# Kernel tuning notes

Measured on AMD Instinct MI355X. Metric: run time of the kernel, lower is better.

Reference implementation:

```python
import jax, jax.numpy as jnp
import numpy as np

B, T, S, H, V, E = 32, 256, 32, 512, 128, 512


def setup_inputs() -> dict:
    key = jax.random.key(0)
    ks = jax.random.split(key, 20)
    f = lambda i, shape: jax.random.normal(ks[i], shape, jnp.float32) * 0.05
    return dict(
        embedding=f(0, (V, H)),
        scope_enc=f(1, (B, S, H)),
        spec_enc=f(2, (B, E)),
        W_init=f(3, (H, E)), b_init=jnp.zeros((H,), jnp.float32),
        W_ih=f(4, (3 * H, 2 * H)), W_hh=f(5, (3 * H, H)),
        b_ih=jnp.zeros((3 * H,), jnp.float32), b_hh=jnp.zeros((3 * H,), jnp.float32),
        W_out=f(6, (V, H)), b_out=jnp.zeros((V,), jnp.float32),
        Wd=f(7, (H, H)), We=f(8, (H, H)), v_attn=f(9, (H,)),
        tokens_in=jax.random.randint(ks[10], (B, T), 0, V),
        tokens_out=jax.random.randint(ks[11], (B, T), 0, V),
        pointer_ids=jax.random.randint(ks[12], (B, T), 0, S),
        ptr_targets=jax.random.randint(ks[13], (B, T), 0, S),
        pointer_mask=jax.random.bernoulli(ks[14], 0.25, (B, T)),
    )


def _gru(x_proj, h0, W_hh, b_hh):
    # x_proj: [B,T,3H] precomputed input projection; torch GRU gate order (r,z,n)
    def step(h, xp):
        gh = h @ W_hh.T + b_hh
        xr, xz, xn = jnp.split(xp, 3, axis=-1)
        hr, hz, hn = jnp.split(gh, 3, axis=-1)
        r = jax.nn.sigmoid(xr + hr)
        z = jax.nn.sigmoid(xz + hz)
        n = jnp.tanh(xn + r * hn)
        h_new = (1.0 - z) * n + z * h
        return h_new, h_new
    _, outs = jax.lax.scan(step, h0, jnp.swapaxes(x_proj, 0, 1))
    return jnp.swapaxes(outs, 0, 1)  # [B,T,H]


def reference(embedding, scope_enc, spec_enc, W_init, b_init, W_ih, W_hh, b_ih, b_hh,
              W_out, b_out, Wd, We, v_attn,
              tokens_in, tokens_out, pointer_ids, ptr_targets, pointer_mask):
    h0 = spec_enc @ W_init.T + b_init                      # initialState
    x_emb = embedding[tokens_in]                           # [B,T,H]
    obj = jax.vmap(lambda s, i: s[i])(scope_enc, pointer_ids)  # [B,T,H]
    obj = jnp.where(pointer_mask[:, :, None], obj, 0.0)    # objectInputs (zeros for non-pointers)
    x = jnp.concatenate([x_emb, obj], axis=-1)             # [B,T,2H]
    x_proj = x @ W_ih.T + b_ih                             # [B,T,3H]
    o = _gru(x_proj, h0, W_hh, b_hh)                       # decoder states [B,T,H]

    # token log-likelihood: -nll_loss(log_softmax(output(o)), targets), summed
    logp = jax.nn.log_softmax(o @ W_out.T + b_out, axis=-1)
    tok_ll = jnp.take_along_axis(logp, tokens_out[:, :, None], axis=-1)[..., 0].sum(-1)

    # pointer attention: additive attention with tanh, log_softmax over scope
    hd = o @ Wd.T                                          # decoderToPointer [B,T,H]
    ok = scope_enc @ We.T                                  # encoderToPointer [B,S,H]
    att = jnp.tanh(hd[:, :, None, :] + ok[:, None, :, :]) @ v_attn  # [B,T,S]
    logatt = jax.nn.log_softmax(att, axis=-1)
    ptr_ll = jnp.take_along_axis(logatt, ptr_targets[:, :, None], axis=-1)[..., 0]
    ptr_ll = jnp.where(pointer_mask, ptr_ll, 0.0).sum(-1)

    return tok_ll + ptr_ll  # per-program likelihood [B]
```

## Files before the change

kernel.cpp:

```cpp
#include <hip/hip_runtime.h>
#include <stdint.h>

#define NB 32
#define NT 256
#define NS 32
#define NH 512
#define NV 128
#define BT 8192

typedef __attribute__((ext_vector_type(8))) __bf16 bf16x8;
typedef __attribute__((ext_vector_type(4))) float f32x4;
typedef __attribute__((ext_vector_type(2))) _Float16 half2v;
typedef unsigned long long u64;

typedef __attribute__((address_space(1))) const unsigned int GASU;
typedef __attribute__((address_space(3))) unsigned int LASU;
#define ASYNC16(g, l) __builtin_amdgcn_global_load_lds((GASU*)(g), (LASU*)(l), 16, 0, 0)

__device__ __forceinline__ half2v pkrtz(float a, float b){
  return __builtin_bit_cast(half2v, __builtin_amdgcn_cvt_pkrtz(a, b));
}
__device__ __forceinline__ unsigned short f2bf(float f){
  unsigned int u = __builtin_bit_cast(unsigned int, f);
  u += 0x7fffu + ((u >> 16) & 1u);
  return (unsigned short)(u >> 16);
}
__device__ __forceinline__ float bf2f(unsigned short h){
  return __builtin_bit_cast(float, ((unsigned int)h) << 16);
}
__device__ __forceinline__ float fexp(float x){ return __builtin_amdgcn_exp2f(x * 1.4426950408889634f); }
__device__ __forceinline__ float fsigm(float x){ return __builtin_amdgcn_rcpf(1.f + fexp(-x)); }
__device__ __forceinline__ float ftanh(float x){
  float t = __builtin_amdgcn_exp2f(x * 2.8853900817779268f);
  return (t - 1.f) * __builtin_amdgcn_rcpf(t + 1.f);
}
__device__ __forceinline__ float flog(float x){ return __builtin_amdgcn_logf(x) * 0.6931471805599453f; }

__device__ __forceinline__ void st_l2(u64* p, u64 v){
  asm volatile("global_store_dwordx2 %0, %1, off" :: "v"(p), "v"(v) : "memory");
}

#define BAR() do{ \
  asm volatile("s_waitcnt lgkmcnt(0)" ::: "memory"); \
  __builtin_amdgcn_sched_barrier(0); \
  __builtin_amdgcn_s_barrier(); \
  __builtin_amdgcn_sched_barrier(0); \
}while(0)

__global__ void k_prep(const float* __restrict__ emb, const float* __restrict__ scope,
                       const float* __restrict__ Wih, const float* __restrict__ Wout,
                       const float* __restrict__ Wd,  const float* __restrict__ We,
                       unsigned short* e_o, unsigned short* s_o, unsigned short* wi_o,
                       unsigned short* wo_o, unsigned short* wd_o, unsigned short* we_o,
                       u64* hx, u64* hxL, float* out){
  int g = blockIdx.x*256 + threadIdx.x, gs = gridDim.x*256;
  if (g < 2*NB*256){
    hx[g] = 0ull;
    __hip_atomic_store(hxL + g, 0ull, __ATOMIC_RELAXED, __HIP_MEMORY_SCOPE_AGENT);
  }
  if (g < NB) out[g] = 0.f;
  for (int i=g; i<NV*NH;      i+=gs) e_o[i]  = f2bf(emb[i]);
  for (int i=g; i<NB*NS*NH;   i+=gs) s_o[i]  = f2bf(scope[i]);
  for (int i=g; i<3*NH*2*NH;  i+=gs) wi_o[i] = f2bf(Wih[i]);
  for (int i=g; i<NV*NH;      i+=gs) wo_o[i] = f2bf(Wout[i]);
  for (int i=g; i<NH*NH;      i+=gs) wd_o[i] = f2bf(Wd[i]);
  for (int i=g; i<NH*NH;      i+=gs) we_o[i] = f2bf(We[i]);
}

__global__ void k_h0(const float* __restrict__ spec, const float* __restrict__ Winit,
                     const float* __restrict__ binit, float* __restrict__ h032,
                     u64* __restrict__ hx, u64* __restrict__ hxL){
  const int b = blockIdx.x, tid = threadIdx.x, lane = tid & 63, w = tid >> 6;
  __shared__ float sp[NH];
  __shared__ float hres[NH];
  if (tid < 128) *(float4*)&sp[tid*4] = *(const float4*)(spec + b*NH + tid*4);
  __syncthreads();
  for (int i = 0; i < 128; ++i){
    int j = w * 128 + i;
    const float4* wr = (const float4*)(Winit + (size_t)j * NH);
    float4 x0 = wr[lane*2], x1 = wr[lane*2 + 1];
    float p = x0.x*sp[lane*8]   + x0.y*sp[lane*8+1] + x0.z*sp[lane*8+2] + x0.w*sp[lane*8+3]
            + x1.x*sp[lane*8+4] + x1.y*sp[lane*8+5] + x1.z*sp[lane*8+6] + x1.w*sp[lane*8+7];
    #pragma unroll
    for (int o = 1; o < 64; o <<= 1) p += __shfl_xor(p, o);
    if (lane == 0){
      float v = p + binit[j];
      h032[b*NH + j] = v;
      hres[j] = v;
    }
  }
  __syncthreads();
  if (tid < 256){
    unsigned int pw = __builtin_bit_cast(unsigned int, pkrtz(hres[2*tid], hres[2*tid+1]));
    u64 pv = (1ull << 32) | (u64)pw;
    __hip_atomic_store(hx + b*256 + tid, pv, __ATOMIC_RELAXED, __HIP_MEMORY_SCOPE_AGENT);
    __hip_atomic_store(hxL + b*256 + tid, pv, __ATOMIC_RELAXED, __HIP_MEMORY_SCOPE_AGENT);
  }
}

__global__ __launch_bounds__(256, 2) void k_gemm(
    const unsigned short* __restrict__ A, const unsigned short* __restrict__ Bw,
    float* __restrict__ Cf, unsigned short* __restrict__ Cbf,
    const float* __restrict__ bias, int M, int N, int K, int ldb)
{
  __shared__ unsigned short lA[2][128][64];
  __shared__ unsigned short lB[2][128][64];
  const int tid = threadIdx.x, lane = tid & 63, wv = tid >> 6;
  const int m0 = blockIdx.x * 128, n0 = blockIdx.y * 128;

  const unsigned short* srcA[4];
  const unsigned short* srcB[4];
  #pragma unroll
  for (int i = 0; i < 4; ++i){
    int ar = m0 + wv*32 + i*8 + (lane >> 3);
    int chunk = (lane & 7) * 8;
    srcA[i] = A + (size_t)ar * K + chunk;
    int br = n0 + wv*32 + i*8 + (lane >> 3);
    srcB[i] = Bw + (size_t)br * ldb + chunk;
  }

  f32x4 acc[4][4];
  #pragma unroll
  for (int x=0;x<4;++x)
    #pragma unroll
    for (int y=0;y<4;++y) acc[x][y] = (f32x4){0.f,0.f,0.f,0.f};

  auto STAGE = [&](int bf, int kt){
    const int k0 = kt * 64;
    #pragma unroll
    for (int i = 0; i < 4; ++i){
      ASYNC16(srcA[i] + k0, &lA[bf][wv*32 + i*8][0]);
      ASYNC16(srcB[i] + k0, &lB[bf][wv*32 + i*8][0]);
    }
  };

  STAGE(0, 0);
  asm volatile("s_waitcnt vmcnt(0)" ::: "memory");
  __syncthreads();

  const int wm = (wv >> 1) * 64, wn = (wv & 1) * 64;
  const int fr = lane & 15, fq = lane >> 4;
  const int nt = K >> 6;
  int cur = 0;
  for (int kt = 0; kt < nt; ++kt){
    if (kt + 1 < nt) STAGE(cur ^ 1, kt + 1);
    #pragma unroll
    for (int ks = 0; ks < 2; ++ks){
      bf16x8 af[4], bfv[4];
      #pragma unroll
      for (int mi = 0; mi < 4; ++mi)
        af[mi] = *(const bf16x8*)&lA[cur][wm + mi*16 + fr][ks*32 + fq*8];
      #pragma unroll
      for (int ni = 0; ni < 4; ++ni)
        bfv[ni] = *(const bf16x8*)&lB[cur][wn + ni*16 + fr][ks*32 + fq*8];
      #pragma unroll
      for (int mi = 0; mi < 4; ++mi)
        #pragma unroll
        for (int ni = 0; ni < 4; ++ni)
          acc[mi][ni] = __builtin_amdgcn_mfma_f32_16x16x32_bf16(af[mi], bfv[ni], acc[mi][ni], 0, 0, 0);
    }
    asm volatile("s_waitcnt vmcnt(0)" ::: "memory");
    __syncthreads();
    cur ^= 1;
  }

  #pragma unroll
  for (int mi = 0; mi < 4; ++mi){
    #pragma unroll
    for (int ni = 0; ni < 4; ++ni){
      int col = n0 + wn + ni*16 + fr;
      float bv = bias ? bias[col] : 0.f;
      #pragma unroll
      for (int rr = 0; rr < 4; ++rr){
        int row = m0 + wm + mi*16 + fq*4 + rr;
        float v = acc[mi][ni][rr] + bv;
        if (Cbf) Cbf[(size_t)row * N + col] = f2bf(v);
        else     Cf [(size_t)row * N + col] = v;
      }
    }
  }
}

__global__ __launch_bounds__(256, 2) void k_logll(
    const unsigned short* __restrict__ A, const unsigned short* __restrict__ Bw,
    const float* __restrict__ bias, const int* __restrict__ tko,
    float* __restrict__ out)
{
  __shared__ unsigned short lA[2][128][64];
  __shared__ unsigned short lB[2][128][64];
  __shared__ float pmax[128][2], psum[128][2], tgt[128], part[2];
  const int tid = threadIdx.x, lane = tid & 63, wv = tid >> 6;
  const int m0 = blockIdx.x * 128;

  const unsigned short* srcA[4];
  const unsigned short* srcB[4];
  #pragma unroll
  for (int i = 0; i < 4; ++i){
    int ar = m0 + wv*32 + i*8 + (lane >> 3);
    int chunk = (lane & 7) * 8;
    srcA[i] = A + (size_t)ar * NH + chunk;
    int br = wv*32 + i*8 + (lane >> 3);
    srcB[i] = Bw + (size_t)br * NH + chunk;
  }

  f32x4 acc[4][4];
  #pragma unroll
  for (int x=0;x<4;++x)
    #pragma unroll
    for (int y=0;y<4;++y) acc[x][y] = (f32x4){0.f,0.f,0.f,0.f};

  auto STAGE = [&](int bf, int kt){
    const int k0 = kt * 64;
    #pragma unroll
    for (int i = 0; i < 4; ++i){
      ASYNC16(srcA[i] + k0, &lA[bf][wv*32 + i*8][0]);
      ASYNC16(srcB[i] + k0, &lB[bf][wv*32 + i*8][0]);
    }
  };

  STAGE(0, 0);
  asm volatile("s_waitcnt vmcnt(0)" ::: "memory");
  __syncthreads();

  const int wm = (wv >> 1) * 64, wn = (wv & 1) * 64;
  const int fr = lane & 15, fq = lane >> 4;
  int cur = 0;
  for (int kt = 0; kt < 8; ++kt){
    if (kt + 1 < 8) STAGE(cur ^ 1, kt + 1);
    #pragma unroll
    for (int ks = 0; ks < 2; ++ks){
      bf16x8 af[4], bfv[4];
      #pragma unroll
      for (int mi = 0; mi < 4; ++mi)
        af[mi] = *(const bf16x8*)&lA[cur][wm + mi*16 + fr][ks*32 + fq*8];
      #pragma unroll
      for (int ni = 0; ni < 4; ++ni)
        bfv[ni] = *(const bf16x8*)&lB[cur][wn + ni*16 + fr][ks*32 + fq*8];
      #pragma unroll
      for (int mi = 0; mi < 4; ++mi)
        #pragma unroll
        for (int ni = 0; ni < 4; ++ni)
          acc[mi][ni] = __builtin_amdgcn_mfma_f32_16x16x32_bf16(af[mi], bfv[ni], acc[mi][ni], 0, 0, 0);
    }
    asm volatile("s_waitcnt vmcnt(0)" ::: "memory");
    __syncthreads();
    cur ^= 1;
  }

  float bv[4];
  #pragma unroll
  for (int ni = 0; ni < 4; ++ni) bv[ni] = bias[wn + ni*16 + fr];
  #pragma unroll
  for (int mi = 0; mi < 4; ++mi){
    #pragma unroll
    for (int rr = 0; rr < 4; ++rr){
      const int rowL = wm + mi*16 + fq*4 + rr;
      float v[4];
      #pragma unroll
      for (int ni = 0; ni < 4; ++ni) v[ni] = acc[mi][ni][rr] + bv[ni];
      int tk = tko[m0 + rowL];
      int rel = tk - wn;
      if (rel >= 0 && rel < 64 && fr == (rel & 15)) tgt[rowL] = v[rel >> 4];
      float m = fmaxf(fmaxf(v[0], v[1]), fmaxf(v[2], v[3]));
      #pragma unroll
      for (int o = 1; o < 16; o <<= 1) m = fmaxf(m, __shfl_xor(m, o));
      float sm = fexp(v[0]-m) + fexp(v[1]-m) + fexp(v[2]-m) + fexp(v[3]-m);
      #pragma unroll
      for (int o = 1; o < 16; o <<= 1) sm += __shfl_xor(sm, o);
      if (fr == 0){ pmax[rowL][wv & 1] = m; psum[rowL][wv & 1] = sm; }
    }
  }
  __syncthreads();
  if (tid < 128){
    float m0h = pmax[tid][0], m1h = pmax[tid][1];
    float M = fmaxf(m0h, m1h);
    float S = psum[tid][0]*fexp(m0h - M) + psum[tid][1]*fexp(m1h - M);
    float ll = tgt[tid] - (M + flog(S));
    #pragma unroll
    for (int o = 1; o < 64; o <<= 1) ll += __shfl_xor(ll, o);
    if ((tid & 63) == 0) part[tid >> 6] = ll;
  }
  __syncthreads();
  if (tid == 0) atomicAdd(out + (m0 >> 8), part[0] + part[1]);
}

__global__ __launch_bounds__(512, 1) void k_gru(
    const float* __restrict__ Whh, const float* __restrict__ bhh,
    const unsigned short* __restrict__ embp,
    const unsigned short* __restrict__ objp,
    const int* __restrict__ tokin, const int* __restrict__ pids,
    const int* __restrict__ pmask,
    const float* __restrict__ h032,
    u64* __restrict__ hx,
    u64* __restrict__ hxL,
    unsigned short* __restrict__ obf)
{
  const int bid = blockIdx.x;
  const int b = bid & 31, s = bid >> 5;
  const int tid = threadIdx.x;
  const int u = tid >> 3, r = tid & 7;
  const int jg = s * 64 + u;

  __shared__ __align__(16) unsigned int hl[256];
  __shared__ float xpl[192];
  __shared__ unsigned int pkb[32];

  half2v w0[8][4], w1[8][4], w2[8][4];
  #pragma unroll
  for (int c = 0; c < 8; ++c){
    const int kb = r*64 + ((c + r) & 7) * 8;
    const float* p0 = Whh + ((size_t)(       jg)) * NH + kb;
    const float* p1 = Whh + ((size_t)(  NH + jg)) * NH + kb;
    const float* p2 = Whh + ((size_t)(2*NH + jg)) * NH + kb;
    #pragma unroll
    for (int p = 0; p < 4; ++p){
      float2 a = *(const float2*)(p0 + 2*p);
      float2 c2 = *(const float2*)(p1 + 2*p);
      float2 d = *(const float2*)(p2 + 2*p);
      w0[c][p] = pkrtz(a.x, a.y);
      w1[c][p] = pkrtz(c2.x, c2.y);
      w2[c][p] = pkrtz(d.x, d.y);
    }
  }
  const float bh0 = bhh[jg], bh1 = bhh[NH + jg], bh2 = bhh[2*NH + jg];
  float hprev = h032[b*NH + jg];

  unsigned short xe = 0, xo = 0; int mk = 0;
  int jcol = 0;
  if (tid >= 256 && tid < 448){
    int idx = tid - 256;
    jcol = (idx >> 6) * NH + s*64 + (idx & 63);
    int tk = tokin[b*NT + 0];
    int pd = pids [b*NT + 0];
    mk     = pmask[b*NT + 0];
    xe = embp[(size_t)tk * 1536 + jcol];
    xo = objp[((size_t)(b*NS + pd)) * 1536 + jcol];
  }
  __syncthreads();

  for (int t = 0; t < NT; ++t){
    if (tid < 256){
      const int base = (((t & 1) * NB + b) << 8) + tid;
      const u64* pL = hxL + base;
      const u64* pM = hx + base;
      const unsigned int want = (unsigned int)(t + 1);
      u64 v;
      u64 a  = __hip_atomic_load(pL, __ATOMIC_RELAXED, __HIP_MEMORY_SCOPE_AGENT);
      u64 b2 = __hip_atomic_load(pL, __ATOMIC_RELAXED, __HIP_MEMORY_SCOPE_AGENT);
      int it = 0;
      while (true){
        if ((unsigned int)(a >> 32) == want){ v = a; break; }
        a = b2;
        b2 = __hip_atomic_load(pL, __ATOMIC_RELAXED, __HIP_MEMORY_SCOPE_AGENT);
        if (((++it) & 7) == 0){
          u64 m = __hip_atomic_load(pM, __ATOMIC_RELAXED, __HIP_MEMORY_SCOPE_AGENT);
          if ((unsigned int)(m >> 32) == want){ v = m; break; }
        }
      }
      hl[tid] = (unsigned int)v;
    } else if (tid < 448){
      int idx = tid - 256;
      xpl[idx] = bf2f(xe) + (mk ? bf2f(xo) : 0.f);
      if (t + 1 < NT){
        int tk = tokin[b*NT + t + 1];
        int pd = pids [b*NT + t + 1];
        mk     = pmask[b*NT + t + 1];
        xe = embp[(size_t)tk * 1536 + jcol];
        xo = objp[((size_t)(b*NS + pd)) * 1536 + jcol];
      }
    }
    BAR();

    float a0 = 0.f, a1 = 0.f, a2 = 0.f;
    half2v hch[8][4];
    #pragma unroll
    for (int c = 0; c < 8; ++c){
      const int g = (r << 3) + ((c + r) & 7);
      uint4 hv = *(const uint4*)&hl[g * 4];
      hch[c][0] = __builtin_bit_cast(half2v, hv.x);
      hch[c][1] = __builtin_bit_cast(half2v, hv.y);
      hch[c][2] = __builtin_bit_cast(half2v, hv.z);
      hch[c][3] = __builtin_bit_cast(half2v, hv.w);
    }
    #pragma unroll
    for (int c = 0; c < 8; ++c){
      #pragma unroll
      for (int p = 0; p < 4; ++p){
        a0 = __builtin_amdgcn_fdot2(w0[c][p], hch[c][p], a0, false);
        a1 = __builtin_amdgcn_fdot2(w1[c][p], hch[c][p], a1, false);
        a2 = __builtin_amdgcn_fdot2(w2[c][p], hch[c][p], a2, false);
      }
    }
    a0 += __shfl_xor(a0, 1); a0 += __shfl_xor(a0, 2); a0 += __shfl_xor(a0, 4);
    a1 += __shfl_xor(a1, 1); a1 += __shfl_xor(a1, 2); a1 += __shfl_xor(a1, 4);
    a2 += __shfl_xor(a2, 1); a2 += __shfl_xor(a2, 2); a2 += __shfl_xor(a2, 4);

    float hnew = 0.f;
    if (r == 0){
      float xr = xpl[u], xz = xpl[64 + u], xn = xpl[128 + u];
      float rg = fsigm(xr + a0 + bh0);
      float zg = fsigm(xz + a1 + bh1);
      float ng = ftanh(xn + rg * (a2 + bh2));
      hnew = (1.f - zg) * ng + zg * hprev;
      hprev = hnew;
    }
    float hpart = __shfl_xor(hnew, 8);
    if (r == 0 && (u & 1) == 0){
      unsigned int pw = __builtin_bit_cast(unsigned int, pkrtz(hnew, hpart));
      u64 pv = ((u64)(unsigned int)(t + 2) << 32) | (u64)pw;
      const int dst = ((((t + 1) & 1) * NB + b) << 8) + (s << 5) + (u >> 1);
      st_l2(hxL + dst, pv);
      __hip_atomic_store(hx + dst, pv,
                         __ATOMIC_RELAXED, __HIP_MEMORY_SCOPE_AGENT);
      pkb[u >> 1] = (unsigned int)f2bf(hnew) | ((unsigned int)f2bf(hpart) << 16);
    }
    BAR();

    if (tid >= 448 && tid < 480){
      int i = tid - 448;
      ((unsigned int*)obf)[((size_t)(b*NT + t)) * (NH/2) + s*32 + i] = pkb[i];
    }
  }
}

__global__ __launch_bounds__(256, 2) void k_ptr(
    const unsigned short* __restrict__ hd, const float* __restrict__ okp,
    const float* __restrict__ vat, const int* __restrict__ ptg,
    const int* __restrict__ pmask, float* __restrict__ out)
{
  __shared__ unsigned short okl[NS][518];
  __shared__ unsigned short hdl[16][518];
  __shared__ float vl[NH];
  __shared__ float attl[16][33];
  const int tid = threadIdx.x;
  const int b = blockIdx.x >> 4, t0 = (blockIdx.x & 15) * 16;
  for (int ii = 0; ii < 64; ++ii){
    int lin = ii*256 + tid;
    int s = lin >> 9, h = lin & 511;
    okl[s][h] = f2bf(okp[((size_t)(b*NS + s)) * NH + h]);
  }
  for (int ii = 0; ii < 32; ++ii){
    int lin = ii*256 + tid;
    int tt = lin >> 9, h = lin & 511;
    hdl[tt][h] = hd[((size_t)(b*NT + t0 + tt)) * NH + h];
  }
  vl[tid] = vat[tid]; vl[256 + tid] = vat[256 + tid];
  __syncthreads();
  #pragma unroll
  for (int pp = 0; pp < 2; ++pp){
    int p = pp*256 + tid;
    int tt = p >> 5, s = p & 31;
    float a = 0.f;
    #pragma unroll 4
    for (int h = 0; h < NH; ++h)
      a += vl[h] * ftanh(bf2f(hdl[tt][h]) + bf2f(okl[s][h]));
    attl[tt][s] = a;
  }
  __syncthreads();
  if (tid < 16){
    int tt = tid;
    float m = -1e30f;
    for (int s = 0; s < NS; ++s) m = fmaxf(m, attl[tt][s]);
    float sm = 0.f;
    for (int s = 0; s < NS; ++s) sm += fexp(attl[tt][s] - m);
    float lse = m + flog(sm);
    int g = b*NT + t0 + tt;
    float c = pmask[g] ? (attl[tt][ptg[g]] - lse) : 0.f;
    #pragma unroll
    for (int o = 1; o < 16; o <<= 1) c += __shfl_xor(c, o);
    if (tid == 0) atomicAdd(out + b, c);
  }
}

extern "C" void kernel_launch(void* const* d_in, const int* in_sizes, int n_in,
                              void* d_out, int out_size, void* d_ws, size_t ws_size,
                              hipStream_t stream)
{
  (void)in_sizes; (void)n_in; (void)out_size; (void)ws_size;
  const float* embedding  = (const float*)d_in[0];
  const float* scope_enc  = (const float*)d_in[1];
  const float* spec_enc   = (const float*)d_in[2];
  const float* W_init     = (const float*)d_in[3];
  const float* b_init     = (const float*)d_in[4];
  const float* W_ih       = (const float*)d_in[5];
  const float* W_hh       = (const float*)d_in[6];
  const float* b_ih       = (const float*)d_in[7];
  const float* b_hh       = (const float*)d_in[8];
  const float* W_out      = (const float*)d_in[9];
  const float* b_out      = (const float*)d_in[10];
  const float* Wd         = (const float*)d_in[11];
  const float* We         = (const float*)d_in[12];
  const float* v_attn     = (const float*)d_in[13];
  const int* tokens_in    = (const int*)d_in[14];
  const int* tokens_out   = (const int*)d_in[15];
  const int* pointer_ids  = (const int*)d_in[16];
  const int* ptr_targets  = (const int*)d_in[17];
  const int* pointer_mask = (const int*)d_in[18];
  float* outF = (float*)d_out;

  uint8_t* wp = (uint8_t*)d_ws;
  auto carve = [&](size_t bytes)->void*{
    void* p = (void*)wp; wp += (bytes + 255) & ~(size_t)255; return p;
  };
  unsigned short* embp_bf  = (unsigned short*)carve((size_t)NV*1536*2);
  unsigned short* objp_bf  = (unsigned short*)carve((size_t)NB*NS*1536*2);
  unsigned short* o_bf     = (unsigned short*)carve((size_t)BT*NH*2);
  unsigned short* hd_bf    = (unsigned short*)carve((size_t)BT*NH*2);
  float*          okp      = (float*)carve((size_t)NB*NS*NH*4);
  unsigned short* emb_bf   = (unsigned short*)carve((size_t)NV*NH*2);
  unsigned short* scope_bf = (unsigned short*)carve((size_t)NB*NS*NH*2);
  unsigned short* Wih_bf   = (unsigned short*)carve((size_t)3*NH*2*NH*2);
  unsigned short* Wout_bf  = (unsigned short*)carve((size_t)NV*NH*2);
  unsigned short* Wd_bf    = (unsigned short*)carve((size_t)NH*NH*2);
  unsigned short* We_bf    = (unsigned short*)carve((size_t)NH*NH*2);
  float*          h032     = (float*)carve((size_t)NB*NH*4);
  u64*            hx       = (u64*)carve((size_t)2*NB*256*8);
  u64*            hxL      = (u64*)carve((size_t)2*NB*256*8);

  hipLaunchKernelGGL(k_prep, dim3(1024), dim3(256), 0, stream,
                     embedding, scope_enc, W_ih, W_out, Wd, We,
                     emb_bf, scope_bf, Wih_bf, Wout_bf, Wd_bf, We_bf,
                     hx, hxL, outF);
  hipLaunchKernelGGL(k_h0, dim3(NB), dim3(256), 0, stream, spec_enc, W_init, b_init,
                     h032, hx, hxL);
  hipLaunchKernelGGL(k_gemm, dim3(1,12), dim3(256), 0, stream,
                     emb_bf, Wih_bf, (float*)nullptr, embp_bf,
                     b_ih, NV, 1536, NH, 1024);
  hipLaunchKernelGGL(k_gemm, dim3(8,12), dim3(256), 0, stream,
                     scope_bf, Wih_bf + NH, (float*)nullptr, objp_bf,
                     (const float*)nullptr, NB*NS, 1536, NH, 1024);
  hipLaunchKernelGGL(k_gru, dim3(256), dim3(512), 0, stream,
                     W_hh, b_hh, embp_bf, objp_bf, tokens_in, pointer_ids,
                     pointer_mask, h032, hx, hxL, o_bf);
  hipLaunchKernelGGL(k_logll, dim3(64), dim3(256), 0, stream,
                     o_bf, Wout_bf, b_out, tokens_out, outF);
  hipLaunchKernelGGL(k_gemm, dim3(64,4), dim3(256), 0, stream,
                     o_bf, Wd_bf, (float*)nullptr, hd_bf, (const float*)nullptr,
                     BT, NH, NH, NH);
  hipLaunchKernelGGL(k_gemm, dim3(8,4), dim3(256), 0, stream,
                     scope_bf, We_bf, okp, (unsigned short*)nullptr,
                     (const float*)nullptr, NB*NS, NH, NH, NH);
  hipLaunchKernelGGL(k_ptr, dim3(512), dim3(256), 0, stream,
                     hd_bf, okp, v_attn, ptr_targets, pointer_mask, outF);
}
```

Baseline: 563.2 us.

## Fuse decoder-to-pointer projection GEMM into pointer attention kernel

```diff
diff --git a/kernel.cpp b/kernel.cpp
--- a/kernel.cpp
+++ b/kernel.cpp
@@ -424,28 +424,59 @@
 }
 
 __global__ __launch_bounds__(256, 2) void k_ptr(
-    const unsigned short* __restrict__ hd, const float* __restrict__ okp,
+    const unsigned short* __restrict__ o_bf, const unsigned short* __restrict__ Wd,
+    const float* __restrict__ okp,
     const float* __restrict__ vat, const int* __restrict__ ptg,
     const int* __restrict__ pmask, float* __restrict__ out)
 {
+  __shared__ unsigned short oA[16][520];
+  __shared__ unsigned short hdl[16][518];
   __shared__ unsigned short okl[NS][518];
-  __shared__ unsigned short hdl[16][518];
   __shared__ float vl[NH];
   __shared__ float attl[16][33];
-  const int tid = threadIdx.x;
+  const int tid = threadIdx.x, lane = tid & 63, wv = tid >> 6;
   const int b = blockIdx.x >> 4, t0 = (blockIdx.x & 15) * 16;
+
+  #pragma unroll
+  for (int ii = 0; ii < 2; ++ii){
+    int lin = ii*256 + tid;
+    int row = lin >> 5, col = (lin & 31) * 16;
+    const uint4* src = (const uint4*)(o_bf + ((size_t)(b*NT + t0 + row)) * NH + col);
+    *(uint4*)&oA[row][col]     = src[0];
+    *(uint4*)&oA[row][col + 8] = src[1];
+  }
   for (int ii = 0; ii < 64; ++ii){
     int lin = ii*256 + tid;
     int s = lin >> 9, h = lin & 511;
     okl[s][h] = f2bf(okp[((size_t)(b*NS + s)) * NH + h]);
   }
-  for (int ii = 0; ii < 32; ++ii){
-    int lin = ii*256 + tid;
-    int tt = lin >> 9, h = lin & 511;
-    hdl[tt][h] = hd[((size_t)(b*NT + t0 + tt)) * NH + h];
-  }
   vl[tid] = vat[tid]; vl[256 + tid] = vat[256 + tid];
   __syncthreads();
+
+  {
+    const int fr = lane & 15, fq = lane >> 4;
+    f32x4 acc[8];
+    #pragma unroll
+    for (int nt = 0; nt < 8; ++nt) acc[nt] = (f32x4){0.f,0.f,0.f,0.f};
+    for (int kt = 0; kt < 16; ++kt){
+      bf16x8 aF = *(const bf16x8*)&oA[fr][kt*32 + fq*8];
+      #pragma unroll
+      for (int nt = 0; nt < 8; ++nt){
+        int brow = wv*128 + nt*16 + fr;
+        bf16x8 bF = *(const bf16x8*)(Wd + (size_t)brow * NH + kt*32 + fq*8);
+        acc[nt] = __builtin_amdgcn_mfma_f32_16x16x32_bf16(aF, bF, acc[nt], 0, 0, 0);
+      }
+    }
+    #pragma unroll
+    for (int nt = 0; nt < 8; ++nt){
+      int col = wv*128 + nt*16 + fr;
+      #pragma unroll
+      for (int rr = 0; rr < 4; ++rr)
+        hdl[fq*4 + rr][col] = f2bf(acc[nt][rr]);
+    }
+  }
+  __syncthreads();
+
   #pragma unroll
   for (int pp = 0; pp < 2; ++pp){
     int p = pp*256 + tid;
@@ -505,7 +536,6 @@
   unsigned short* embp_bf  = (unsigned short*)carve((size_t)NV*1536*2);
   unsigned short* objp_bf  = (unsigned short*)carve((size_t)NB*NS*1536*2);
   unsigned short* o_bf     = (unsigned short*)carve((size_t)BT*NH*2);
-  unsigned short* hd_bf    = (unsigned short*)carve((size_t)BT*NH*2);
   float*          okp      = (float*)carve((size_t)NB*NS*NH*4);
   unsigned short* emb_bf   = (unsigned short*)carve((size_t)NV*NH*2);
   unsigned short* scope_bf = (unsigned short*)carve((size_t)NB*NS*NH*2);
@@ -529,17 +559,14 @@
   hipLaunchKernelGGL(k_gemm, dim3(8,12), dim3(256), 0, stream,
                      scope_bf, Wih_bf + NH, (float*)nullptr, objp_bf,
                      (const float*)nullptr, NB*NS, 1536, NH, 1024);
+  hipLaunchKernelGGL(k_gemm, dim3(8,4), dim3(256), 0, stream,
+                     scope_bf, We_bf, okp, (unsigned short*)nullptr,
+                     (const float*)nullptr, NB*NS, NH, NH, NH);
   hipLaunchKernelGGL(k_gru, dim3(256), dim3(512), 0, stream,
                      W_hh, b_hh, embp_bf, objp_bf, tokens_in, pointer_ids,
                      pointer_mask, h032, hx, hxL, o_bf);
   hipLaunchKernelGGL(k_logll, dim3(64), dim3(256), 0, stream,
                      o_bf, Wout_bf, b_out, tokens_out, outF);
-  hipLaunchKernelGGL(k_gemm, dim3(64,4), dim3(256), 0, stream,
-                     o_bf, Wd_bf, (float*)nullptr, hd_bf, (const float*)nullptr,
-                     BT, NH, NH, NH);
-  hipLaunchKernelGGL(k_gemm, dim3(8,4), dim3(256), 0, stream,
-                     scope_bf, We_bf, okp, (unsigned short*)nullptr,
-                     (const float*)nullptr, NB*NS, NH, NH, NH);
   hipLaunchKernelGGL(k_ptr, dim3(512), dim3(256), 0, stream,
-                     hd_bf, okp, v_attn, ptr_targets, pointer_mask, outF);
-}
+                     o_bf, Wd_bf, okp, v_attn, ptr_targets, pointer_mask, outF);
+}
```

After: 597.2 us. 1.06x slower.

## Merge GEMM launches and place GRU blocks on XCDs by batch group

Applied to the files above, without the earlier changes.

```diff
diff --git a/kernel.cpp b/kernel.cpp
--- a/kernel.cpp
+++ b/kernel.cpp
@@ -47,17 +47,200 @@
   __builtin_amdgcn_sched_barrier(0); \
 }while(0)
 
+struct SmemGemm { unsigned short lA[2][128][64]; unsigned short lB[2][128][64]; };
+struct SmemLog  { SmemGemm g; float pmax[128][2]; float psum[128][2]; float tgt[128]; float part[2]; };
+
+__device__ __forceinline__ void gemm_core(
+    SmemGemm& sm, const unsigned short* __restrict__ A,
+    const unsigned short* __restrict__ Bw,
+    float* __restrict__ Cf, unsigned short* __restrict__ Cbf,
+    const float* __restrict__ bias, int N, int K, int ldb, int m0, int n0)
+{
+  const int tid = threadIdx.x, lane = tid & 63, wv = tid >> 6;
+  const unsigned short* srcA[4];
+  const unsigned short* srcB[4];
+  #pragma unroll
+  for (int i = 0; i < 4; ++i){
+    int ar = m0 + wv*32 + i*8 + (lane >> 3);
+    int chunk = (lane & 7) * 8;
+    srcA[i] = A + (size_t)ar * K + chunk;
+    int br = n0 + wv*32 + i*8 + (lane >> 3);
+    srcB[i] = Bw + (size_t)br * ldb + chunk;
+  }
+
+  f32x4 acc[4][4];
+  #pragma unroll
+  for (int x=0;x<4;++x)
+    #pragma unroll
+    for (int y=0;y<4;++y) acc[x][y] = (f32x4){0.f,0.f,0.f,0.f};
+
+  auto STAGE = [&](int bf, int kt){
+    const int k0 = kt * 64;
+    #pragma unroll
+    for (int i = 0; i < 4; ++i){
+      ASYNC16(srcA[i] + k0, &sm.lA[bf][wv*32 + i*8][0]);
+      ASYNC16(srcB[i] + k0, &sm.lB[bf][wv*32 + i*8][0]);
+    }
+  };
+
+  STAGE(0, 0);
+  asm volatile("s_waitcnt vmcnt(0)" ::: "memory");
+  __syncthreads();
+
+  const int wm = (wv >> 1) * 64, wn = (wv & 1) * 64;
+  const int fr = lane & 15, fq = lane >> 4;
+  const int nt = K >> 6;
+  int cur = 0;
+  for (int kt = 0; kt < nt; ++kt){
+    if (kt + 1 < nt) STAGE(cur ^ 1, kt + 1);
+    #pragma unroll
+    for (int ks = 0; ks < 2; ++ks){
+      bf16x8 af[4], bfv[4];
+      #pragma unroll
+      for (int mi = 0; mi < 4; ++mi)
+        af[mi] = *(const bf16x8*)&sm.lA[cur][wm + mi*16 + fr][ks*32 + fq*8];
+      #pragma unroll
+      for (int ni = 0; ni < 4; ++ni)
+        bfv[ni] = *(const bf16x8*)&sm.lB[cur][wn + ni*16 + fr][ks*32 + fq*8];
+      #pragma unroll
+      for (int mi = 0; mi < 4; ++mi)
+        #pragma unroll
+        for (int ni = 0; ni < 4; ++ni)
+          acc[mi][ni] = __builtin_amdgcn_mfma_f32_16x16x32_bf16(af[mi], bfv[ni], acc[mi][ni], 0, 0, 0);
+    }
+    asm volatile("s_waitcnt vmcnt(0)" ::: "memory");
+    __syncthreads();
+    cur ^= 1;
+  }
+
+  #pragma unroll
+  for (int mi = 0; mi < 4; ++mi){
+    #pragma unroll
+    for (int ni = 0; ni < 4; ++ni){
+      int col = n0 + wn + ni*16 + fr;
+      float bv = bias ? bias[col] : 0.f;
+      #pragma unroll
+      for (int rr = 0; rr < 4; ++rr){
+        int row = m0 + wm + mi*16 + fq*4 + rr;
+        float v = acc[mi][ni][rr] + bv;
+        if (Cbf) Cbf[(size_t)row * N + col] = f2bf(v);
+        else     Cf [(size_t)row * N + col] = v;
+      }
+    }
+  }
+}
+
+__device__ __forceinline__ void logll_core(
+    SmemLog& sm, const unsigned short* __restrict__ A,
+    const unsigned short* __restrict__ Bw,
+    const float* __restrict__ bias, const int* __restrict__ tko,
+    float* __restrict__ out, int m0)
+{
+  const int tid = threadIdx.x, lane = tid & 63, wv = tid >> 6;
+  const unsigned short* srcA[4];
+  const unsigned short* srcB[4];
+  #pragma unroll
+  for (int i = 0; i < 4; ++i){
+    int ar = m0 + wv*32 + i*8 + (lane >> 3);
+    int chunk = (lane & 7) * 8;
+    srcA[i] = A + (size_t)ar * NH + chunk;
+    int br = wv*32 + i*8 + (lane >> 3);
+    srcB[i] = Bw + (size_t)br * NH + chunk;
+  }
+
+  f32x4 acc[4][4];
+  #pragma unroll
+  for (int x=0;x<4;++x)
+    #pragma unroll
+    for (int y=0;y<4;++y) acc[x][y] = (f32x4){0.f,0.f,0.f,0.f};
+
+  auto STAGE = [&](int bf, int kt){
+    const int k0 = kt * 64;
+    #pragma unroll
+    for (int i = 0; i < 4; ++i){
+      ASYNC16(srcA[i] + k0, &sm.g.lA[bf][wv*32 + i*8][0]);
+      ASYNC16(srcB[i] + k0, &sm.g.lB[bf][wv*32 + i*8][0]);
+    }
+  };
+
+  STAGE(0, 0);
+  asm volatile("s_waitcnt vmcnt(0)" ::: "memory");
+  __syncthreads();
+
+  const int wm = (wv >> 1) * 64, wn = (wv & 1) * 64;
+  const int fr = lane & 15, fq = lane >> 4;
+  int cur = 0;
+  for (int kt = 0; kt < 8; ++kt){
+    if (kt + 1 < 8) STAGE(cur ^ 1, kt + 1);
+    #pragma unroll
+    for (int ks = 0; ks < 2; ++ks){
+      bf16x8 af[4], bfv[4];
+      #pragma unroll
+      for (int mi = 0; mi < 4; ++mi)
+        af[mi] = *(const bf16x8*)&sm.g.lA[cur][wm + mi*16 + fr][ks*32 + fq*8];
+      #pragma unroll
+      for (int ni = 0; ni < 4; ++ni)
+        bfv[ni] = *(const bf16x8*)&sm.g.lB[cur][wn + ni*16 + fr][ks*32 + fq*8];
+      #pragma unroll
+      for (int mi = 0; mi < 4; ++mi)
+        #pragma unroll
+        for (int ni = 0; ni < 4; ++ni)
+          acc[mi][ni] = __builtin_amdgcn_mfma_f32_16x16x32_bf16(af[mi], bfv[ni], acc[mi][ni], 0, 0, 0);
+    }
+    asm volatile("s_waitcnt vmcnt(0)" ::: "memory");
+    __syncthreads();
+    cur ^= 1;
+  }
+
+  float bv[4];
+  #pragma unroll
+  for (int ni = 0; ni < 4; ++ni) bv[ni] = bias[wn + ni*16 + fr];
+  #pragma unroll
+  for (int mi = 0; mi < 4; ++mi){
+    #pragma unroll
+    for (int rr = 0; rr < 4; ++rr){
+      const int rowL = wm + mi*16 + fq*4 + rr;
+      float v[4];
+      #pragma unroll
+      for (int ni = 0; ni < 4; ++ni) v[ni] = acc[mi][ni][rr] + bv[ni];
+      int tk = tko[m0 + rowL];
+      int rel = tk - wn;
+      if (rel >= 0 && rel < 64 && fr == (rel & 15)) sm.tgt[rowL] = v[rel >> 4];
+      float m = fmaxf(fmaxf(v[0], v[1]), fmaxf(v[2], v[3]));
+      #pragma unroll
+      for (int o = 1; o < 16; o <<= 1) m = fmaxf(m, __shfl_xor(m, o));
+      float s = fexp(v[0]-m) + fexp(v[1]-m) + fexp(v[2]-m) + fexp(v[3]-m);
+      #pragma unroll
+      for (int o = 1; o < 16; o <<= 1) s += __shfl_xor(s, o);
+      if (fr == 0){ sm.pmax[rowL][wv & 1] = m; sm.psum[rowL][wv & 1] = s; }
+    }
+  }
+  __syncthreads();
+  if (tid < 128){
+    float m0h = sm.pmax[tid][0], m1h = sm.pmax[tid][1];
+    float M = fmaxf(m0h, m1h);
+    float S = sm.psum[tid][0]*fexp(m0h - M) + sm.psum[tid][1]*fexp(m1h - M);
+    float ll = sm.tgt[tid] - (M + flog(S));
+    #pragma unroll
+    for (int o = 1; o < 64; o <<= 1) ll += __shfl_xor(ll, o);
+    if ((tid & 63) == 0) sm.part[tid >> 6] = ll;
+  }
+  __syncthreads();
+  if (tid == 0) atomicAdd(out + (m0 >> 8), sm.part[0] + sm.part[1]);
+}
+
 __global__ void k_prep(const float* __restrict__ emb, const float* __restrict__ scope,
                        const float* __restrict__ Wih, const float* __restrict__ Wout,
                        const float* __restrict__ Wd,  const float* __restrict__ We,
                        unsigned short* e_o, unsigned short* s_o, unsigned short* wi_o,
                        unsigned short* wo_o, unsigned short* wd_o, unsigned short* we_o,
-                       u64* hx, u64* hxL, float* out){
+                       u64* hx, u64* hxL, int* claim, float* out){
   int g = blockIdx.x*256 + threadIdx.x, gs = gridDim.x*256;
   if (g < 2*NB*256){
     hx[g] = 0ull;
     __hip_atomic_store(hxL + g, 0ull, __ATOMIC_RELAXED, __HIP_MEMORY_SCOPE_AGENT);
   }
+  if (g < 16) __hip_atomic_store(claim + g, 0, __ATOMIC_RELAXED, __HIP_MEMORY_SCOPE_AGENT);
   if (g < NB) out[g] = 0.f;
   for (int i=g; i<NV*NH;      i+=gs) e_o[i]  = f2bf(emb[i]);
   for (int i=g; i<NB*NS*NH;   i+=gs) s_o[i]  = f2bf(scope[i]);
@@ -98,190 +281,43 @@
   }
 }
 
-__global__ __launch_bounds__(256, 2) void k_gemm(
-    const unsigned short* __restrict__ A, const unsigned short* __restrict__ Bw,
-    float* __restrict__ Cf, unsigned short* __restrict__ Cbf,
-    const float* __restrict__ bias, int M, int N, int K, int ldb)
-{
-  __shared__ unsigned short lA[2][128][64];
-  __shared__ unsigned short lB[2][128][64];
-  const int tid = threadIdx.x, lane = tid & 63, wv = tid >> 6;
-  const int m0 = blockIdx.x * 128, n0 = blockIdx.y * 128;
-
-  const unsigned short* srcA[4];
-  const unsigned short* srcB[4];
-  #pragma unroll
-  for (int i = 0; i < 4; ++i){
-    int ar = m0 + wv*32 + i*8 + (lane >> 3);
-    int chunk = (lane & 7) * 8;
-    srcA[i] = A + (size_t)ar * K + chunk;
-    int br = n0 + wv*32 + i*8 + (lane >> 3);
-    srcB[i] = Bw + (size_t)br * ldb + chunk;
-  }
-
-  f32x4 acc[4][4];
-  #pragma unroll
-  for (int x=0;x<4;++x)
-    #pragma unroll
-    for (int y=0;y<4;++y) acc[x][y] = (f32x4){0.f,0.f,0.f,0.f};
-
-  auto STAGE = [&](int bf, int kt){
-    const int k0 = kt * 64;
-    #pragma unroll
-    for (int i = 0; i < 4; ++i){
-      ASYNC16(srcA[i] + k0, &lA[bf][wv*32 + i*8][0]);
-      ASYNC16(srcB[i] + k0, &lB[bf][wv*32 + i*8][0]);
-    }
-  };
-
-  STAGE(0, 0);
-  asm volatile("s_waitcnt vmcnt(0)" ::: "memory");
-  __syncthreads();
-
-  const int wm = (wv >> 1) * 64, wn = (wv & 1) * 64;
-  const int fr = lane & 15, fq = lane >> 4;
-  const int nt = K >> 6;
-  int cur = 0;
-  for (int kt = 0; kt < nt; ++kt){
-    if (kt + 1 < nt) STAGE(cur ^ 1, kt + 1);
-    #pragma unroll
-    for (int ks = 0; ks < 2; ++ks){
-      bf16x8 af[4], bfv[4];
-      #pragma unroll
-      for (int mi = 0; mi < 4; ++mi)
-        af[mi] = *(const bf16x8*)&lA[cur][wm + mi*16 + fr][ks*32 + fq*8];
-      #pragma unroll
-      for (int ni = 0; ni < 4; ++ni)
-        bfv[ni] = *(const bf16x8*)&lB[cur][wn + ni*16 + fr][ks*32 + fq*8];
-      #pragma unroll
-      for (int mi = 0; mi < 4; ++mi)
-        #pragma unroll
-        for (int ni = 0; ni < 4; ++ni)
-          acc[mi][ni] = __builtin_amdgcn_mfma_f32_16x16x32_bf16(af[mi], bfv[ni], acc[mi][ni], 0, 0, 0);
-    }
-    asm volatile("s_waitcnt vmcnt(0)" ::: "memory");
-    __syncthreads();
-    cur ^= 1;
-  }
-
-  #pragma unroll
-  for (int mi = 0; mi < 4; ++mi){
-    #pragma unroll
-    for (int ni = 0; ni < 4; ++ni){
-      int col = n0 + wn + ni*16 + fr;
-      float bv = bias ? bias[col] : 0.f;
-      #pragma unroll
-      for (int rr = 0; rr < 4; ++rr){
-        int row = m0 + wm + mi*16 + fq*4 + rr;
-        float v = acc[mi][ni][rr] + bv;
-        if (Cbf) Cbf[(size_t)row * N + col] = f2bf(v);
-        else     Cf [(size_t)row * N + col] = v;
-      }
-    }
-  }
-}
-
-__global__ __launch_bounds__(256, 2) void k_logll(
-    const unsigned short* __restrict__ A, const unsigned short* __restrict__ Bw,
-    const float* __restrict__ bias, const int* __restrict__ tko,
-    float* __restrict__ out)
-{
-  __shared__ unsigned short lA[2][128][64];
-  __shared__ unsigned short lB[2][128][64];
-  __shared__ float pmax[128][2], psum[128][2], tgt[128], part[2];
-  const int tid = threadIdx.x, lane = tid & 63, wv = tid >> 6;
-  const int m0 = blockIdx.x * 128;
-
-  const unsigned short* srcA[4];
-  const unsigned short* srcB[4];
-  #pragma unroll
-  for (int i = 0; i < 4; ++i){
-    int ar = m0 + wv*32 + i*8 + (lane >> 3);
-    int chunk = (lane & 7) * 8;
-    srcA[i] = A + (size_t)ar * NH + chunk;
-    int br = wv*32 + i*8 + (lane >> 3);
-    srcB[i] = Bw + (size_t)br * NH + chunk;
-  }
-
-  f32x4 acc[4][4];
-  #pragma unroll
-  for (int x=0;x<4;++x)
-    #pragma unroll
-    for (int y=0;y<4;++y) acc[x][y] = (f32x4){0.f,0.f,0.f,0.f};
-
-  auto STAGE = [&](int bf, int kt){
-    const int k0 = kt * 64;
-    #pragma unroll
-    for (int i = 0; i < 4; ++i){
-      ASYNC16(srcA[i] + k0, &lA[bf][wv*32 + i*8][0]);
-      ASYNC16(srcB[i] + k0, &lB[bf][wv*32 + i*8][0]);
-    }
-  };
-
-  STAGE(0, 0);
-  asm volatile("s_waitcnt vmcnt(0)" ::: "memory");
-  __syncthreads();
-
-  const int wm = (wv >> 1) * 64, wn = (wv & 1) * 64;
-  const int fr = lane & 15, fq = lane >> 4;
-  int cur = 0;
-  for (int kt = 0; kt < 8; ++kt){
-    if (kt + 1 < 8) STAGE(cur ^ 1, kt + 1);
-    #pragma unroll
-    for (int ks = 0; ks < 2; ++ks){
-      bf16x8 af[4], bfv[4];
-      #pragma unroll
-      for (int mi = 0; mi < 4; ++mi)
-        af[mi] = *(const bf16x8*)&lA[cur][wm + mi*16 + fr][ks*32 + fq*8];
-      #pragma unroll
-      for (int ni = 0; ni < 4; ++ni)
-        bfv[ni] = *(const bf16x8*)&lB[cur][wn + ni*16 + fr][ks*32 + fq*8];
-      #pragma unroll
-      for (int mi = 0; mi < 4; ++mi)
-        #pragma unroll
-        for (int ni = 0; ni < 4; ++ni)
-          acc[mi][ni] = __builtin_amdgcn_mfma_f32_16x16x32_bf16(af[mi], bfv[ni], acc[mi][ni], 0, 0, 0);
-    }
-    asm volatile("s_waitcnt vmcnt(0)" ::: "memory");
-    __syncthreads();
-    cur ^= 1;
-  }
-
-  float bv[4];
-  #pragma unroll
-  for (int ni = 0; ni < 4; ++ni) bv[ni] = bias[wn + ni*16 + fr];
-  #pragma unroll
-  for (int mi = 0; mi < 4; ++mi){
-    #pragma unroll
-    for (int rr = 0; rr < 4; ++rr){
-      const int rowL = wm + mi*16 + fq*4 + rr;
-      float v[4];
-      #pragma unroll
-      for (int ni = 0; ni < 4; ++ni) v[ni] = acc[mi][ni][rr] + bv[ni];
-      int tk = tko[m0 + rowL];
-      int rel = tk - wn;
-      if (rel >= 0 && rel < 64 && fr == (rel & 15)) tgt[rowL] = v[rel >> 4];
-      float m = fmaxf(fmaxf(v[0], v[1]), fmaxf(v[2], v[3]));
-      #pragma unroll
-      for (int o = 1; o < 16; o <<= 1) m = fmaxf(m, __shfl_xor(m, o));
-      float sm = fexp(v[0]-m) + fexp(v[1]-m) + fexp(v[2]-m) + fexp(v[3]-m);
-      #pragma unroll
-      for (int o = 1; o < 16; o <<= 1) sm += __shfl_xor(sm, o);
-      if (fr == 0){ pmax[rowL][wv & 1] = m; psum[rowL][wv & 1] = sm; }
-    }
-  }
-  __syncthreads();
-  if (tid < 128){
-    float m0h = pmax[tid][0], m1h = pmax[tid][1];
-    float M = fmaxf(m0h, m1h);
-    float S = psum[tid][0]*fexp(m0h - M) + psum[tid][1]*fexp(m1h - M);
-    float ll = tgt[tid] - (M + flog(S));
-    #pragma unroll
-    for (int o = 1; o < 64; o <<= 1) ll += __shfl_xor(ll, o);
-    if ((tid & 63) == 0) part[tid >> 6] = ll;
-  }
-  __syncthreads();
-  if (tid == 0) atomicAdd(out + (m0 >> 8), part[0] + part[1]);
+__global__ __launch_bounds__(256, 2) void k_pre(
+    const unsigned short* __restrict__ emb_bf, const unsigned short* __restrict__ scope_bf,
+    const unsigned short* __restrict__ Wih_bf, const unsigned short* __restrict__ We_bf,
+    const float* __restrict__ b_ih,
+    unsigned short* __restrict__ embp, unsigned short* __restrict__ objp,
+    float* __restrict__ okp)
+{
+  __shared__ SmemGemm sm;
+  const int blk = blockIdx.x;
+  if (blk < 12){
+    gemm_core(sm, emb_bf, Wih_bf, nullptr, embp, b_ih, 1536, NH, 1024, 0, blk*128);
+  } else if (blk < 108){
+    int i = blk - 12;
+    gemm_core(sm, scope_bf, Wih_bf + NH, nullptr, objp, nullptr, 1536, NH, 1024,
+              (i/12)*128, (i%12)*128);
+  } else {
+    int i = blk - 108;
+    gemm_core(sm, scope_bf, We_bf, okp, nullptr, nullptr, NH, NH, NH,
+              (i/4)*128, (i%4)*128);
+  }
+}
+
+__global__ __launch_bounds__(256, 2) void k_tail(
+    const unsigned short* __restrict__ o_bf, const unsigned short* __restrict__ Wout_bf,
+    const float* __restrict__ b_out, const int* __restrict__ tko,
+    float* __restrict__ out,
+    const unsigned short* __restrict__ Wd_bf, unsigned short* __restrict__ hd_bf)
+{
+  __shared__ SmemLog sm;
+  const int blk = blockIdx.x;
+  if (blk < 64){
+    logll_core(sm, o_bf, Wout_bf, b_out, tko, out, blk*128);
+  } else {
+    int i = blk - 64;
+    gemm_core(sm.g, o_bf, Wd_bf, nullptr, hd_bf, nullptr, NH, NH, NH,
+              (i/4)*128, (i%4)*128);
+  }
 }
 
 __global__ __launch_bounds__(512, 1) void k_gru(
@@ -293,11 +329,33 @@
     const float* __restrict__ h032,
     u64* __restrict__ hx,
     u64* __restrict__ hxL,
+    int* __restrict__ claim,
     unsigned short* __restrict__ obf)
 {
-  const int bid = blockIdx.x;
-  const int b = bid & 31, s = bid >> 5;
   const int tid = threadIdx.x;
+  __shared__ int slotS;
+  if (tid == 0){
+    unsigned int xcd;
+    asm volatile("s_getreg_b32 %0, hwreg(HW_REG_XCC_ID)" : "=s"(xcd));
+    xcd &= 7;
+    int idx = atomicAdd(claim + xcd, 1);
+    int slot;
+    if (idx < 32) slot = (int)(xcd << 5) + idx;
+    else {
+      slot = -1;
+      #pragma unroll 1
+      for (int k = 1; k < 8 && slot < 0; ++k){
+        int x = (int)((xcd + k) & 7);
+        int j = atomicAdd(claim + x, 1);
+        if (j < 32) slot = (x << 5) + j;
+      }
+    }
+    slotS = slot;
+  }
+  __syncthreads();
+  const int slot = slotS;
+  const int b = ((slot >> 5) << 2) | ((slot >> 3) & 3);
+  const int s = slot & 7;
   const int u = tid >> 3, r = tid & 7;
   const int jg = s * 64 + u;
 
@@ -516,30 +574,22 @@
   float*          h032     = (float*)carve((size_t)NB*NH*4);
   u64*            hx       = (u64*)carve((size_t)2*NB*256*8);
   u64*            hxL      = (u64*)carve((size_t)2*NB*256*8);
+  int*            claim    = (int*)carve(1024);
 
   hipLaunchKernelGGL(k_prep, dim3(1024), dim3(256), 0, stream,
                      embedding, scope_enc, W_ih, W_out, Wd, We,
                      emb_bf, scope_bf, Wih_bf, Wout_bf, Wd_bf, We_bf,
-                     hx, hxL, outF);
+                     hx, hxL, claim, outF);
   hipLaunchKernelGGL(k_h0, dim3(NB), dim3(256), 0, stream, spec_enc, W_init, b_init,
                      h032, hx, hxL);
-  hipLaunchKernelGGL(k_gemm, dim3(1,12), dim3(256), 0, stream,
-                     emb_bf, Wih_bf, (float*)nullptr, embp_bf,
-                     b_ih, NV, 1536, NH, 1024);
-  hipLaunchKernelGGL(k_gemm, dim3(8,12), dim3(256), 0, stream,
-                     scope_bf, Wih_bf + NH, (float*)nullptr, objp_bf,
-                     (const float*)nullptr, NB*NS, 1536, NH, 1024);
+  hipLaunchKernelGGL(k_pre, dim3(140), dim3(256), 0, stream,
+                     emb_bf, scope_bf, Wih_bf, We_bf, b_ih,
+                     embp_bf, objp_bf, okp);
   hipLaunchKernelGGL(k_gru, dim3(256), dim3(512), 0, stream,
                      W_hh, b_hh, embp_bf, objp_bf, tokens_in, pointer_ids,
-                     pointer_mask, h032, hx, hxL, o_bf);
-  hipLaunchKernelGGL(k_logll, dim3(64), dim3(256), 0, stream,
-                     o_bf, Wout_bf, b_out, tokens_out, outF);
-  hipLaunchKernelGGL(k_gemm, dim3(64,4), dim3(256), 0, stream,
-                     o_bf, Wd_bf, (float*)nullptr, hd_bf, (const float*)nullptr,
-                     BT, NH, NH, NH);
-  hipLaunchKernelGGL(k_gemm, dim3(8,4), dim3(256), 0, stream,
-                     scope_bf, We_bf, okp, (unsigned short*)nullptr,
-                     (const float*)nullptr, NB*NS, NH, NH, NH);
+                     pointer_mask, h032, hx, hxL, claim, o_bf);
+  hipLaunchKernelGGL(k_tail, dim3(320), dim3(256), 0, stream,
+                     o_bf, Wout_bf, b_out, tokens_out, outF, Wd_bf, hd_bf);
   hipLaunchKernelGGL(k_ptr, dim3(512), dim3(256), 0, stream,
                      hd_bf, okp, v_attn, ptr_targets, pointer_mask, outF);
 }
```

Measured after the change: 587.4 us. 1.04x slower.
